# Kernel tuning notes

Measured on AMD Instinct MI355X. Metric: run time of the kernel, lower is better.

Reference implementation:

```python
import jax, jax.numpy as jnp
import numpy as np

# GMM generation labels (non-contiguous FreeSurfer-style values), as in __init__
GEN_LABELS = np.array([0, 2, 3, 4, 5, 7, 8, 10, 11, 12, 13, 14, 15, 16, 17, 18,
                       24, 26, 28, 41, 42, 43, 44, 46, 47], dtype=np.int32)
N_LABELS = len(GEN_LABELS)            # 25
MAX_LABEL = int(GEN_LABELS.max()) + 1  # 48
B, D, H, W, C = 2, 160, 160, 160, 2


def setup_inputs() -> dict:
    key = jax.random.key(0)
    k1, k2, k3, k4 = jax.random.split(key, 4)
    # label_map values must lie in GEN_LABELS: draw indices then map to label values
    idx = jax.random.randint(k1, (B, D, H, W, 1), 0, N_LABELS)
    label_map = jnp.asarray(GEN_LABELS)[idx].astype(jnp.int32)
    means = jax.random.normal(k2, (B, N_LABELS, C), dtype=jnp.float32)
    stds = jax.random.uniform(k3, (B, N_LABELS, C), dtype=jnp.float32)
    # tf.random.normal(tf.shape(labels)) materialized as an explicit input
    noise = jax.random.normal(k4, (B, D, H, W, C), dtype=jnp.float32)
    return {"label_map": label_map, "means": means, "stds": stds, "noise": noise}


def reference(label_map, means, stds, noise):
    # Inverse lookup table: label value -> row index into means/stds.
    # This replaces the per-channel scatter_nd table + per-batch map_fn gather
    # of the original with a single batched gather (same math).
    lut = jnp.zeros((MAX_LABEL,), jnp.int32).at[jnp.asarray(GEN_LABELS)].set(
        jnp.arange(N_LABELS, dtype=jnp.int32))
    idx = lut[label_map[..., 0]]                      # [B, D, H, W]
    flat = idx.reshape(idx.shape[0], -1)              # [B, V]
    c = means.shape[-1]
    means_map = jnp.take_along_axis(means, flat[:, :, None], axis=1)
    means_map = means_map.reshape(*idx.shape, c)      # [B, D, H, W, C]
    stds_map = jnp.take_along_axis(stds, flat[:, :, None], axis=1)
    stds_map = stds_map.reshape(*idx.shape, c)        # [B, D, H, W, C]
    return stds_map * noise + means_map
```

## Files before the change

kernel.cpp:

```cpp
#include <hip/hip_runtime.h>

#define VPB   4096000
#define NLAB  25
#define MAXL  48
#define TOTAL_VOX 8192000

__device__ __constant__ int c_lut[MAXL] = {
     0,  0,  1,  2,  3,  4,  0,  5,
     6,  0,  7,  8,  9, 10, 11, 12,
    13, 14, 15,  0,  0,  0,  0,  0,
    16,  0, 17,  0, 18,  0,  0,  0,
     0,  0,  0,  0,  0,  0,  0,  0,
     0, 19, 20, 21, 22,  0, 23, 24
};

__global__ __launch_bounds__(256) void gmm_sample_kernel(
    const int*   __restrict__ labels,
    const float* __restrict__ means,
    const float* __restrict__ stds,
    const float* __restrict__ noise,
    float*       __restrict__ out)
{
    __shared__ float4 table[2 * MAXL];

    const int tid = threadIdx.x;
    const int g  = blockIdx.x * 256 + tid;
    const int v0 = g << 2;

    const int4   lab = *(const int4*)  (labels + v0);
    const float4 n0  = *(const float4*)(noise + ((size_t)v0 << 1));
    const float4 n1  = *(const float4*)(noise + ((size_t)v0 << 1) + 4);

    if (tid < 2 * MAXL) {
        const int b = tid / MAXL;
        const int v = tid - b * MAXL;
        const int row = c_lut[v];
        const float* mp = means + ((b * NLAB + row) << 1);
        const float* sp = stds  + ((b * NLAB + row) << 1);
        table[tid] = make_float4(mp[0], mp[1], sp[0], sp[1]);
    }
    __syncthreads();

    const int boff = (v0 >= VPB) ? MAXL : 0;

    const float4 e0 = table[boff + lab.x];
    const float4 e1 = table[boff + lab.y];
    const float4 e2 = table[boff + lab.z];
    const float4 e3 = table[boff + lab.w];

    float4 o0, o1;
    o0.x = fmaf(e0.z, n0.x, e0.x);
    o0.y = fmaf(e0.w, n0.y, e0.y);
    o0.z = fmaf(e1.z, n0.z, e1.x);
    o0.w = fmaf(e1.w, n0.w, e1.y);
    o1.x = fmaf(e2.z, n1.x, e2.x);
    o1.y = fmaf(e2.w, n1.y, e2.y);
    o1.z = fmaf(e3.z, n1.z, e3.x);
    o1.w = fmaf(e3.w, n1.w, e3.y);

    *(float4*)(out + ((size_t)v0 << 1))     = o0;
    *(float4*)(out + ((size_t)v0 << 1) + 4) = o1;
}

extern "C" void kernel_launch(void* const* d_in, const int* in_sizes, int n_in,
                              void* d_out, int out_size, void* d_ws, size_t ws_size,
                              hipStream_t stream) {
    const int*   labels = (const int*)  d_in[0];
    const float* means  = (const float*)d_in[1];
    const float* stds   = (const float*)d_in[2];
    const float* noise  = (const float*)d_in[3];
    float* out = (float*)d_out;

    const int threads = 256;
    const int total_threads = TOTAL_VOX / 4;
    const int blocks = total_threads / threads;
    gmm_sample_kernel<<<blocks, threads, 0, stream>>>(labels, means, stds, noise, out);
}
```

Measured before the change: 142.1 us.

## Process four voxel chunks per thread with register prefetch of next chunk

Each thread now handles four strided chunks of voxels instead of one, and the grid shrinks fourfold. The labels and noise for the next chunk are loaded before computing the current one, so memory loads overlap with compute. This amortizes the per-block LUT/table setup and the barrier. The trade-off is fewer blocks resident on the GPU, which lowers latency hiding from occupancy.

Result: no change. 144.0 us (+1.3%).

```diff
diff --git a/kernel.cpp b/kernel.cpp
--- a/kernel.cpp
+++ b/kernel.cpp
@@ -4,6 +4,9 @@
 #define NLAB  25
 #define MAXL  48
 #define TOTAL_VOX 8192000
+
+#define NTHREADS_TOT 512000
+#define ITER_VOX     2048000
 
 __device__ __constant__ int c_lut[MAXL] = {
      0,  0,  1,  2,  3,  4,  0,  5,
@@ -23,13 +26,13 @@
 {
     __shared__ float4 table[2 * MAXL];
 
-    const int tid = threadIdx.x;
-    const int g  = blockIdx.x * 256 + tid;
-    const int v0 = g << 2;
+    const int tid  = threadIdx.x;
+    const int base = blockIdx.x * 256 + tid;
+    const size_t v0base = (size_t)base << 2;
 
-    const int4   lab = *(const int4*)  (labels + v0);
-    const float4 n0  = *(const float4*)(noise + ((size_t)v0 << 1));
-    const float4 n1  = *(const float4*)(noise + ((size_t)v0 << 1) + 4);
+    int4   lab = *(const int4*)  (labels + v0base);
+    float4 cn0 = *(const float4*)(noise + (v0base << 1));
+    float4 cn1 = *(const float4*)(noise + (v0base << 1) + 4);
 
     if (tid < 2 * MAXL) {
         const int b = tid / MAXL;
@@ -41,25 +44,42 @@
     }
     __syncthreads();
 
-    const int boff = (v0 >= VPB) ? MAXL : 0;
+    #pragma unroll
+    for (int i = 0; i < 4; ++i) {
+        const size_t v0 = v0base + (size_t)i * ITER_VOX;
 
-    const float4 e0 = table[boff + lab.x];
-    const float4 e1 = table[boff + lab.y];
-    const float4 e2 = table[boff + lab.z];
-    const float4 e3 = table[boff + lab.w];
+        const int4   l  = lab;
+        const float4 n0 = cn0;
+        const float4 n1 = cn1;
 
-    float4 o0, o1;
-    o0.x = fmaf(e0.z, n0.x, e0.x);
-    o0.y = fmaf(e0.w, n0.y, e0.y);
-    o0.z = fmaf(e1.z, n0.z, e1.x);
-    o0.w = fmaf(e1.w, n0.w, e1.y);
-    o1.x = fmaf(e2.z, n1.x, e2.x);
-    o1.y = fmaf(e2.w, n1.y, e2.y);
-    o1.z = fmaf(e3.z, n1.z, e3.x);
-    o1.w = fmaf(e3.w, n1.w, e3.y);
+        if (i < 3) {
+            const size_t vn = v0base + (size_t)(i + 1) * ITER_VOX;
+            lab = *(const int4*)  (labels + vn);
+            cn0 = *(const float4*)(noise + (vn << 1));
+            cn1 = *(const float4*)(noise + (vn << 1) + 4);
+        }
 
-    *(float4*)(out + ((size_t)v0 << 1))     = o0;
-    *(float4*)(out + ((size_t)v0 << 1) + 4) = o1;
+        const int boff = (i >= 2) ? MAXL : 0;
+
+        const float4 e0 = table[boff + l.x];
+        const float4 e1 = table[boff + l.y];
+        const float4 e2 = table[boff + l.z];
+        const float4 e3 = table[boff + l.w];
+
+        float4 o0, o1;
+        o0.x = fmaf(e0.z, n0.x, e0.x);
+        o0.y = fmaf(e0.w, n0.y, e0.y);
+        o0.z = fmaf(e1.z, n0.z, e1.x);
+        o0.w = fmaf(e1.w, n0.w, e1.y);
+        o1.x = fmaf(e2.z, n1.x, e2.x);
+        o1.y = fmaf(e2.w, n1.y, e2.y);
+        o1.z = fmaf(e3.z, n1.z, e3.x);
+        o1.w = fmaf(e3.w, n1.w, e3.y);
+
+        float4* op = (float4*)(out + (v0 << 1));
+        op[0] = o0;
+        op[1] = o1;
+    }
 }
 
 extern "C" void kernel_launch(void* const* d_in, const int* in_sizes, int n_in,
@@ -72,7 +92,6 @@
     float* out = (float*)d_out;
 
     const int threads = 256;
-    const int total_threads = TOTAL_VOX / 4;
-    const int blocks = total_threads / threads;
+    const int blocks = NTHREADS_TOT / threads;
     gmm_sample_kernel<<<blocks, threads, 0, stream>>>(labels, means, stds, noise, out);
 }
```
